# Performance work log

Hardware: AMD Instinct MI355X
Metric: run time of the kernel (lower is better)

## Reference

```python
import jax, jax.numpy as jnp
import numpy as np

B, C_IN, IMG = 16, 3, 224
P = 8                      # patch size (kernel == stride)
D = 256                    # d_model == embed_dim
NH = 8                     # num heads
HD = D // NH               # head dim = 32
G = IMG // P               # 28x28 patch grid
N = G * G                  # 784 patches
MRD = 31                   # max_relative_dist
T = 2 * MRD - 1            # 61
SCALE = HD ** -0.5


def setup_inputs() -> dict:
    key = jax.random.key(0)
    ks = jax.random.split(key, 11)
    std = 0.02
    yy, xx = jnp.meshgrid(jnp.arange(G), jnp.arange(G), indexing='ij')
    pos = jnp.stack([yy.ravel(), xx.ravel()], axis=-1).astype(jnp.int32)  # (N,2)
    return {
        'cur_frame': jax.random.normal(ks[0], (B, C_IN, IMG, IMG), jnp.float32),
        'prev_frame': jax.random.normal(ks[1], (B, C_IN, IMG, IMG), jnp.float32),
        'conv_w': jax.random.normal(ks[2], (D, C_IN, P, P), jnp.float32) * std,
        'conv_b': jnp.zeros((D,), jnp.float32),
        'q_w': jax.random.normal(ks[3], (D, D), jnp.float32) * std,
        'q_b': jnp.zeros((D,), jnp.float32),
        'kv_w': jax.random.normal(ks[4], (2 * D, D), jnp.float32) * std,
        'kv_b': jnp.zeros((2 * D,), jnp.float32),
        'proj_w': jax.random.normal(ks[5], (D, D), jnp.float32) * std,
        'proj_b': jnp.zeros((D,), jnp.float32),
        'bias_table': jax.random.normal(ks[6], (T * T, NH), jnp.float32) * std,
        'cur_pos': pos,
        'prev_pos': pos,
    }


def _patch_embed(x, w, b):
    # Conv2d with kernel==stride==P (non-overlapping patches)
    y = jax.lax.conv_general_dilated(
        x, w, window_strides=(P, P), padding='VALID',
        dimension_numbers=('NCHW', 'OIHW', 'NCHW'))
    y = y + b[None, :, None, None]
    Bb, Dd, h, wd = y.shape
    return y.reshape(Bb, Dd, h * wd).transpose(0, 2, 1)  # (B, N, D)


def reference(cur_frame, prev_frame, conv_w, conv_b, q_w, q_b, kv_w, kv_b,
              proj_w, proj_b, bias_table, cur_pos, prev_pos):
    cur = _patch_embed(cur_frame, conv_w, conv_b)    # (B, N, D)
    prev = _patch_embed(prev_frame, conv_w, conv_b)  # (B, N, D)

    q = (cur @ q_w.T + q_b).reshape(B, N, NH, HD).transpose(0, 2, 1, 3) * SCALE
    kv = prev @ kv_w.T + kv_b                        # (B, N, 2D)
    k = kv[..., :D].reshape(B, N, NH, HD).transpose(0, 2, 1, 3)
    v = kv[..., D:].reshape(B, N, NH, HD).transpose(0, 2, 1, 3)

    attn = jnp.einsum('bhqd,bhkd->bhqk', q, k)       # (B, NH, N, N)

    # relative position bias gather: idx = (dy+30)*61 + (dx+30)
    rel = cur_pos[:, None, :] - prev_pos[None, :, :]             # (N, N, 2)
    idx = (rel[..., 0] + (MRD - 1)) * T + (rel[..., 1] + (MRD - 1))
    bias = bias_table[idx].transpose(2, 0, 1)                    # (NH, N, N)

    attn = jax.nn.softmax(attn + bias[None], axis=-1)
    x = jnp.einsum('bhqk,bhkd->bqhd', attn, v).reshape(B, N, D)
    return x @ proj_w.T + proj_b
```

## Files before the change

### kernel.cpp

```cpp
#include <hip/hip_runtime.h>

#define B_ 16
#define NP 784
#define D_ 256
#define NH_ 8
#define HD_ 32
#define KEMB 192
#define SCALE_ 0.17677669529663687f
#define LOG2E_ 1.4426950408889634f

typedef __attribute__((ext_vector_type(4))) float f32x4;
typedef __attribute__((ext_vector_type(8))) short bf16x8;
typedef __attribute__((ext_vector_type(4))) short bf16x4;

__device__ __forceinline__ unsigned short f2bf(float f) {
    union { float f; unsigned int u; } v; v.f = f;
    unsigned int u = v.u;
    unsigned int r = (u + 0x7fffu + ((u >> 16) & 1u)) >> 16;
    return (unsigned short)r;
}

__device__ __forceinline__ unsigned int cvtpk(float a, float b) {
    unsigned int r;
    asm("v_cvt_pk_bf16_f32 %0, %1, %2" : "=v"(r) : "v"(a), "v"(b));
    return r;
}

__device__ __forceinline__ float fexp2(float x) {
#if __has_builtin(__builtin_amdgcn_exp2f)
    return __builtin_amdgcn_exp2f(x);
#else
    return exp2f(x);
#endif
}

__device__ __forceinline__ void gl_lds16(const unsigned short* g, unsigned short* l) {
    __builtin_amdgcn_global_load_lds(
        (const __attribute__((address_space(1))) unsigned int*)(const void*)g,
        (__attribute__((address_space(3))) unsigned int*)(void*)l, 16, 0, 0);
}

__global__ __launch_bounds__(256) void prep_k(
    const float* __restrict__ s0, const float* __restrict__ s1,
    const float* __restrict__ s2, const float* __restrict__ s3,
    unsigned short* __restrict__ d,
    const float* __restrict__ bt, float* __restrict__ bto)
{
    if (blockIdx.x < 304) {
        int i = (blockIdx.x * 256 + threadIdx.x) * 4;
        const float* s; int off;
        if (i < 49152)            { s = s0; off = i; }
        else if (i < 114688)      { s = s1; off = i - 49152; }
        else if (i < 245760)      { s = s2; off = i - 114688; }
        else if (i < 311296)      { s = s3; off = i - 245760; }
        else return;
        float4 v = *(const float4*)(s + off);
        unsigned short o0 = f2bf(v.x), o1 = f2bf(v.y), o2 = f2bf(v.z), o3 = f2bf(v.w);
        unsigned short* dst = d + i;
        dst[0] = o0; dst[1] = o1; dst[2] = o2; dst[3] = o3;
    } else {
        int i = (blockIdx.x - 304) * 256 + threadIdx.x;
        if (i < 29768) {
            int h = i / 3721, idx = i - h * 3721;
            bto[i] = bt[idx * NH_ + h] * LOG2E_;
        }
    }
}

__global__ __launch_bounds__(256) void gemm_conv(
    const float* __restrict__ cur, const float* __restrict__ prev,
    const unsigned short* __restrict__ W, const float* __restrict__ bias,
    unsigned short* __restrict__ outp)
{
    __shared__ __align__(16) unsigned short At[32 * 64];
    __shared__ __align__(16) unsigned short Bt[256 * 64];
    const int tid = threadIdx.x;
    const int lane = tid & 63, wid = tid >> 6;
    const int lo = lane & 15, hi = lane >> 4;
    const int m0 = blockIdx.x * 32;
    const int wvb = wid * 512;
    const float* asrc;
    unsigned short* adst;
    {
        int row = tid >> 3, seg = tid & 7;
        int m = m0 + row;
        int fb = m / NP, n = m - fb * NP;
        int py = n / 28, px = n - py * 28;
        const float* F = (fb >= 16 ? prev + (size_t)(fb - 16) * 150528 : cur + (size_t)fb * 150528);
        asrc = F + (py * 8 + seg) * 224 + px * 8;
        adst = At + row * 64 + ((seg ^ (row & 7)) * 8);
    }
    f32x4 acc[2][4] = {};
#pragma unroll
    for (int kt = 0; kt < 3; ++kt) {
        __syncthreads();
#pragma unroll
        for (int i = 0; i < 8; ++i) {
            int s = i * 256 + tid;
            int row = s >> 3, seg = (s & 7) ^ (row & 7);
            gl_lds16(W + (size_t)row * KEMB + kt * 64 + seg * 8, Bt + i * 2048 + wvb);
        }
        {
            const float* src = asrc + kt * 50176;
            float4 a0 = *(const float4*)(src);
            float4 a1 = *(const float4*)(src + 4);
            union { unsigned int u[4]; bf16x8 v; } ov;
            ov.u[0] = cvtpk(a0.x, a0.y); ov.u[1] = cvtpk(a0.z, a0.w);
            ov.u[2] = cvtpk(a1.x, a1.y); ov.u[3] = cvtpk(a1.z, a1.w);
            *(bf16x8*)(void*)(adst) = ov.v;
        }
        __syncthreads();
#pragma unroll
        for (int kk = 0; kk < 2; ++kk) {
            bf16x8 af[2], bfv[4];
#pragma unroll
            for (int f = 0; f < 2; ++f) {
                int rowa = f * 16 + lo;
                af[f] = *(const bf16x8*)(const void*)(At + rowa * 64 + (((kk * 4 + hi) ^ (rowa & 7)) * 8));
            }
#pragma unroll
            for (int f = 0; f < 4; ++f) {
                int rowb = wid * 64 + f * 16 + lo;
                bfv[f] = *(const bf16x8*)(const void*)(Bt + rowb * 64 + (((kk * 4 + hi) ^ (rowb & 7)) * 8));
            }
#pragma unroll
            for (int fr = 0; fr < 2; ++fr)
#pragma unroll
                for (int fc = 0; fc < 4; ++fc)
                    acc[fr][fc] = __builtin_amdgcn_mfma_f32_16x16x32_bf16(af[fr], bfv[fc], acc[fr][fc], 0, 0, 0);
        }
    }
#pragma unroll
    for (int fr = 0; fr < 2; ++fr)
#pragma unroll
        for (int fc = 0; fc < 4; ++fc)
#pragma unroll
            for (int r = 0; r < 4; ++r) {
                int m = m0 + fr * 16 + hi * 4 + r;
                int c = wid * 64 + fc * 16 + lo;
                outp[(size_t)m * D_ + c] = f2bf(acc[fr][fc][r] + bias[c]);
            }
}

__global__ __launch_bounds__(256) void gemm_qkv(
    const unsigned short* __restrict__ emb,
    const unsigned short* __restrict__ w_q, const float* __restrict__ q_b,
    const unsigned short* __restrict__ w_kv, const float* __restrict__ kv_b,
    unsigned short* __restrict__ q_h, unsigned short* __restrict__ k_h,
    unsigned short* __restrict__ v_t)
{
    __shared__ __align__(16) unsigned short At[128 * 64];
    __shared__ __align__(16) unsigned short Bt[128 * 64];
    const int tid = threadIdx.x;
    const int lo = tid & 15, hi = (tid >> 4) & 3, wid = tid >> 6;
    const int m0 = blockIdx.x * 128;
    const int y = blockIdx.y;
    const bool iskv = y >= 2;
    const unsigned short* Abase = iskv ? emb + (size_t)12544 * D_ : emb;
    const unsigned short* W = iskv ? w_kv : w_q;
    const float* bias = iskv ? kv_b : q_b;
    const int n0 = (iskv ? y - 2 : y) * 128;
    const int wr = wid >> 1, wc = wid & 1;
    const int wvb = wid * 512;
    f32x4 acc[4][4] = {};
#pragma unroll
    for (int kt = 0; kt < 4; ++kt) {
        const int k0 = kt * 64;
        __syncthreads();
#pragma unroll
        for (int i = 0; i < 4; ++i) {
            int s = i * 256 + tid;
            int row = s >> 3, seg = (s & 7) ^ (row & 7);
            gl_lds16(Abase + (size_t)(m0 + row) * D_ + k0 + seg * 8, At + i * 2048 + wvb);
            gl_lds16(W + (size_t)(n0 + row) * D_ + k0 + seg * 8, Bt + i * 2048 + wvb);
        }
        __syncthreads();
#pragma unroll
        for (int kk = 0; kk < 2; ++kk) {
            bf16x8 af[4], bfv[4];
#pragma unroll
            for (int f = 0; f < 4; ++f) {
                int rowa = wr * 64 + f * 16 + lo;
                af[f] = *(const bf16x8*)(const void*)(At + rowa * 64 + (((kk * 4 + hi) ^ (rowa & 7)) * 8));
                int rowb = wc * 64 + f * 16 + lo;
                bfv[f] = *(const bf16x8*)(const void*)(Bt + rowb * 64 + (((kk * 4 + hi) ^ (rowb & 7)) * 8));
            }
#pragma unroll
            for (int fr = 0; fr < 4; ++fr)
#pragma unroll
                for (int fc = 0; fc < 4; ++fc)
                    acc[fr][fc] = __builtin_amdgcn_mfma_f32_16x16x32_bf16(af[fr], bfv[fc], acc[fr][fc], 0, 0, 0);
        }
    }
#pragma unroll
    for (int fr = 0; fr < 4; ++fr)
#pragma unroll
        for (int fc = 0; fc < 4; ++fc)
#pragma unroll
            for (int r = 0; r < 4; ++r) {
                int m = m0 + wr * 64 + fr * 16 + hi * 4 + r;
                int c = n0 + wc * 64 + fc * 16 + lo;
                float val = acc[fr][fc][r] + bias[c];
                int b = m / NP, n = m - (m / NP) * NP;
                if (!iskv) {
                    int h = c >> 5, d = c & 31;
                    q_h[(((size_t)(b * NH_ + h)) * NP + n) * HD_ + d] = f2bf(val * (SCALE_ * LOG2E_));
                } else if (c < D_) {
                    int h = c >> 5, d = c & 31;
                    k_h[(((size_t)(b * NH_ + h)) * NP + n) * HD_ + d] = f2bf(val);
                } else {
                    int cc = c - D_; int h = cc >> 5, d = cc & 31;
                    v_t[(((size_t)(b * NH_ + h)) * HD_ + d) * NP + n] = f2bf(val);
                }
            }
}

__global__ __launch_bounds__(256) void gemm_px(
    const unsigned short* __restrict__ A, const unsigned short* __restrict__ W,
    const float* __restrict__ bias, float* __restrict__ outp)
{
    __shared__ __align__(16) unsigned short At[32 * 64];
    __shared__ __align__(16) unsigned short Bt[128 * 64];
    const int tid = threadIdx.x;
    const int lo = tid & 15, hi = (tid >> 4) & 3, wid = tid >> 6;
    const int m0 = blockIdx.x * 32, n0 = blockIdx.y * 128;
    const int wr = wid >> 1, wc = wid & 1;
    const int wvb = wid * 512;
    f32x4 acc[4] = {};
#pragma unroll
    for (int kt = 0; kt < 4; ++kt) {
        const int k0 = kt * 64;
        __syncthreads();
        {
            int row = tid >> 3, seg = (tid & 7) ^ ((tid >> 3) & 7);
            gl_lds16(A + (size_t)(m0 + row) * D_ + k0 + seg * 8, At + wvb);
        }
#pragma unroll
        for (int i = 0; i < 4; ++i) {
            int s = i * 256 + tid;
            int row = s >> 3, seg = (s & 7) ^ (row & 7);
            gl_lds16(W + (size_t)(n0 + row) * D_ + k0 + seg * 8, Bt + i * 2048 + wvb);
        }
        __syncthreads();
#pragma unroll
        for (int kk = 0; kk < 2; ++kk) {
            bf16x8 af, bfv[4];
            {
                int rowa = wr * 16 + lo;
                af = *(const bf16x8*)(const void*)(At + rowa * 64 + (((kk * 4 + hi) ^ (rowa & 7)) * 8));
            }
#pragma unroll
            for (int f = 0; f < 4; ++f) {
                int rowb = wc * 64 + f * 16 + lo;
                bfv[f] = *(const bf16x8*)(const void*)(Bt + rowb * 64 + (((kk * 4 + hi) ^ (rowb & 7)) * 8));
            }
#pragma unroll
            for (int fc = 0; fc < 4; ++fc)
                acc[fc] = __builtin_amdgcn_mfma_f32_16x16x32_bf16(af, bfv[fc], acc[fc], 0, 0, 0);
        }
    }
#pragma unroll
    for (int fc = 0; fc < 4; ++fc)
#pragma unroll
        for (int r = 0; r < 4; ++r) {
            int m = m0 + wr * 16 + hi * 4 + r;
            int c = n0 + wc * 64 + fc * 16 + lo;
            outp[(size_t)m * D_ + c] = acc[fc][r] + bias[c];
        }
}

__global__ __launch_bounds__(448) void attn_k(
    const unsigned short* __restrict__ qh, const unsigned short* __restrict__ kh,
    const unsigned short* __restrict__ vt, const float* __restrict__ bias_t,
    const int* __restrict__ cpos, const int* __restrict__ ppos,
    unsigned short* __restrict__ x)
{
    __shared__ __align__(16) unsigned short Vt[2][32 * 64];
    __shared__ __align__(16) float2 Bp[1890];
    __shared__ int ktab[196];
    const int tid = threadIdx.x;
    const int lane = tid & 63, wid = tid >> 6;
    const int lo = lane & 15, hi = lane >> 4;
    const int bid = blockIdx.x;
    const int h = bid & 7;
    const int t2 = bid >> 3;
    const int b = t2 / 7;
    const int qt = t2 - b * 7;
    const int bh = b * 8 + h;
    const int q0 = qt * 112 + wid * 16;
    const int blbase = (qt * 4 + 3) * 61;

    {
        const float* bsl = bias_t + h * 3721 + blbase;
        for (int i = tid; i < 1890; i += 448)
            Bp[i] = float2{ bsl[i], bsl[i + 1] };
        if (tid < 196) {
            int kc = tid * 4;
            ktab[tid] = ppos[2 * kc] * 61 + ppos[2 * kc + 1];
        }
    }

    bf16x8 qf;
    int qb;
    {
        int qr = q0 + lo;
        qf = *(const bf16x8*)(const void*)(qh + (((size_t)bh * NP) + qr) * HD_ + hi * 8);
        qb = cpos[qr * 2] * 61 + cpos[qr * 2 + 1] + 1860 - blbase;
    }

    const unsigned short* kbase = kh + (size_t)bh * NP * HD_;
    const unsigned short* vbase = vt + (size_t)bh * HD_ * NP;
    const int tv = tid - 192, sd = tv >> 3, ssg = tv & 7;
    bf16x8 vst = {};

    auto issue = [&](int kt) {
        if (tid >= 192)
            vst = *(const bf16x8*)(const void*)(vbase + sd * NP + kt * 64 + ssg * 8);
    };
    auto stage = [&](int buf) {
        if (tid >= 192) {
            int f = ssg >> 2;
            int j4 = ((ssg >> 1) & 1) * 4;
            int blkA = f * 4 + ((2 * ssg) & 3);
            int blkB = f * 4 + ((2 * ssg + 1) & 3);
            bf16x4 vlo = { vst[0], vst[1], vst[2], vst[3] };
            bf16x4 vhi = { vst[4], vst[5], vst[6], vst[7] };
            *(bf16x4*)(void*)(Vt[buf] + sd * 64 + ((blkA ^ (sd & 7)) * 8) + j4) = vlo;
            *(bf16x4*)(void*)(Vt[buf] + sd * 64 + ((blkB ^ (sd & 7)) * 8) + j4) = vhi;
        }
    };

    f32x4 o[2] = {};
    float lr = 0.f;

    issue(0);
    stage(0);
    for (int kt = 0; kt < 13; ++kt) {
        int cur = kt & 1;
        int k0 = kt * 64;
        if (kt < 12) issue(kt + 1);
        bf16x8 kf[4];
#pragma unroll
        for (int g = 0; g < 4; ++g)
            kf[g] = *(const bf16x8*)(const void*)(kbase + (size_t)(k0 + g * 16 + lo) * HD_ + hi * 8);
        __syncthreads();
        bool tail = (kt == 12);

        f32x4 bc[4];
#pragma unroll
        for (int g = 0; g < 4; ++g) {
            if (tail && g > 0) {
                bc[g] = f32x4{ -1e30f, -1e30f, -1e30f, -1e30f };
            } else {
                int kbg = ktab[kt * 16 + g * 4 + hi];
                int off = qb - kbg - 3;
                float2 pA = Bp[off];
                float2 pB = Bp[off + 2];
                bc[g][0] = pB.y; bc[g][1] = pB.x; bc[g][2] = pA.y; bc[g][3] = pA.x;
            }
        }
        f32x4 s[4];
#pragma unroll
        for (int g = 0; g < 4; ++g)
            s[g] = __builtin_amdgcn_mfma_f32_16x16x32_bf16(kf[g], qf, bc[g], 0, 0, 0);
        unsigned int c[4][2];
        float psum = 0.f;
#pragma unroll
        for (int g = 0; g < 4; ++g) {
            float p0 = fexp2(s[g][0]);
            float p1 = fexp2(s[g][1]);
            float p2 = fexp2(s[g][2]);
            float p3 = fexp2(s[g][3]);
            psum += (p0 + p1) + (p2 + p3);
            c[g][0] = cvtpk(p0, p1);
            c[g][1] = cvtpk(p2, p3);
        }
        lr += psum;
#pragma unroll
        for (int f = 0; f < 2; ++f) {
            union { unsigned int u[4]; bf16x8 v; } pu;
            pu.u[0] = c[2 * f][0]; pu.u[1] = c[2 * f][1];
            pu.u[2] = c[2 * f + 1][0]; pu.u[3] = c[2 * f + 1][1];
#pragma unroll
            for (int cc = 0; cc < 2; ++cc) {
                int d = cc * 16 + lo;
                bf16x8 vf = *(const bf16x8*)(const void*)(Vt[cur] + d * 64 + (((f * 4 + hi) ^ (d & 7)) * 8));
                o[cc] = __builtin_amdgcn_mfma_f32_16x16x32_bf16(pu.v, vf, o[cc], 0, 0, 0);
            }
        }
        if (kt < 12) stage(cur ^ 1);
    }
    lr += __shfl_xor(lr, 16);
    lr += __shfl_xor(lr, 32);
    float li = 1.0f / lr;
    float lro[4];
#pragma unroll
    for (int r = 0; r < 4; ++r)
        lro[r] = __shfl(li, (lane & 48) | (hi * 4 + r));
#pragma unroll
    for (int cc = 0; cc < 2; ++cc)
#pragma unroll
        for (int r = 0; r < 4; ++r) {
            int qr = q0 + hi * 4 + r;
            float val = o[cc][r] * lro[r];
            x[((size_t)b * NP + qr) * D_ + h * HD_ + cc * 16 + lo] = f2bf(val);
        }
}

extern "C" void kernel_launch(void* const* d_in, const int* in_sizes, int n_in,
                              void* d_out, int out_size, void* d_ws, size_t ws_size,
                              hipStream_t stream)
{
    const float* cur    = (const float*)d_in[0];
    const float* prev   = (const float*)d_in[1];
    const float* conv_w = (const float*)d_in[2];
    const float* conv_b = (const float*)d_in[3];
    const float* q_w    = (const float*)d_in[4];
    const float* q_b    = (const float*)d_in[5];
    const float* kv_w   = (const float*)d_in[6];
    const float* kv_b   = (const float*)d_in[7];
    const float* proj_w = (const float*)d_in[8];
    const float* proj_b = (const float*)d_in[9];
    const float* btab   = (const float*)d_in[10];
    const int* cpos     = (const int*)d_in[11];
    const int* ppos     = (const int*)d_in[12];

    char* ws = (char*)d_ws;
    unsigned short* w_conv = (unsigned short*)(ws + 0);
    unsigned short* w_q    = (unsigned short*)(ws + 98304);
    unsigned short* w_kv   = (unsigned short*)(ws + 229376);
    unsigned short* w_pr   = (unsigned short*)(ws + 491520);
    float* bias_t          = (float*)(ws + 622592);
    unsigned short* emb    = (unsigned short*)(ws + 10256384);
    unsigned short* q_h    = (unsigned short*)(ws + 23101440);
    unsigned short* k_h    = (unsigned short*)(ws + 29523968);
    unsigned short* v_t    = (unsigned short*)(ws + 35946496);
    unsigned short* xb     = (unsigned short*)(ws + 42369024);

    prep_k<<<421, 256, 0, stream>>>(conv_w, q_w, kv_w, proj_w, w_conv, btab, bias_t);
    gemm_conv<<<784, 256, 0, stream>>>(cur, prev, w_conv, conv_b, emb);
    gemm_qkv<<<dim3(98, 6), 256, 0, stream>>>(emb, w_q, q_b, w_kv, kv_b, q_h, k_h, v_t);
    attn_k<<<896, 448, 0, stream>>>(q_h, k_h, v_t, bias_t, cpos, ppos, xb);
    gemm_px<<<dim3(392, 2), 256, 0, stream>>>(xb, w_pr, proj_b, (float*)d_out);

    (void)in_sizes; (void)n_in; (void)out_size; (void)ws_size;
}
```

Before: 78.87 us.

## Fuse patch-embed conv GEMM with Q/KV projection via LDS-resident embedding tile

Merges the conv patch-embedding GEMM and the Q/KV projection GEMM into one kernel. Each 32-row block keeps its bf16 embedding tile in shared memory and immediately multiplies it by the Q or KV weights, which are read directly from global memory. This removes the emb round-trip through HBM and one kernel launch. In exchange, the 32-row tiles reuse weights less, weight fragments are loaded uncached from global memory inside the MFMA loop, and prev-frame blocks do twice the work of cur-frame blocks, creating load imbalance.

```diff
diff --git a/kernel.cpp b/kernel.cpp
--- a/kernel.cpp
+++ b/kernel.cpp
@@ -67,10 +67,13 @@
     }
 }
 
-__global__ __launch_bounds__(256) void gemm_conv(
+__global__ __launch_bounds__(256) void conv_qkv(
     const float* __restrict__ cur, const float* __restrict__ prev,
-    const unsigned short* __restrict__ W, const float* __restrict__ bias,
-    unsigned short* __restrict__ outp)
+    const unsigned short* __restrict__ W, const float* __restrict__ cbias,
+    const unsigned short* __restrict__ w_q, const float* __restrict__ q_b,
+    const unsigned short* __restrict__ w_kv, const float* __restrict__ kv_b,
+    unsigned short* __restrict__ q_h, unsigned short* __restrict__ k_h,
+    unsigned short* __restrict__ v_t)
 {
     __shared__ __align__(16) unsigned short At[32 * 64];
     __shared__ __align__(16) unsigned short Bt[256 * 64];
@@ -130,89 +133,79 @@
                     acc[fr][fc] = __builtin_amdgcn_mfma_f32_16x16x32_bf16(af[fr], bfv[fc], acc[fr][fc], 0, 0, 0);
         }
     }
+    __syncthreads();
+    unsigned short* Et = Bt;
 #pragma unroll
     for (int fr = 0; fr < 2; ++fr)
 #pragma unroll
         for (int fc = 0; fc < 4; ++fc)
 #pragma unroll
             for (int r = 0; r < 4; ++r) {
-                int m = m0 + fr * 16 + hi * 4 + r;
-                int c = wid * 64 + fc * 16 + lo;
-                outp[(size_t)m * D_ + c] = f2bf(acc[fr][fc][r] + bias[c]);
-            }
-}
-
-__global__ __launch_bounds__(256) void gemm_qkv(
-    const unsigned short* __restrict__ emb,
-    const unsigned short* __restrict__ w_q, const float* __restrict__ q_b,
-    const unsigned short* __restrict__ w_kv, const float* __restrict__ kv_b,
-    unsigned short* __restrict__ q_h, unsigned short* __restrict__ k_h,
-    unsigned short* __restrict__ v_t)
-{
-    __shared__ __align__(16) unsigned short At[128 * 64];
-    __shared__ __align__(16) unsigned short Bt[128 * 64];
-    const int tid = threadIdx.x;
-    const int lo = tid & 15, hi = (tid >> 4) & 3, wid = tid >> 6;
-    const int m0 = blockIdx.x * 128;
-    const int y = blockIdx.y;
-    const bool iskv = y >= 2;
-    const unsigned short* Abase = iskv ? emb + (size_t)12544 * D_ : emb;
-    const unsigned short* W = iskv ? w_kv : w_q;
-    const float* bias = iskv ? kv_b : q_b;
-    const int n0 = (iskv ? y - 2 : y) * 128;
-    const int wr = wid >> 1, wc = wid & 1;
-    const int wvb = wid * 512;
-    f32x4 acc[4][4] = {};
-#pragma unroll
-    for (int kt = 0; kt < 4; ++kt) {
-        const int k0 = kt * 64;
-        __syncthreads();
-#pragma unroll
-        for (int i = 0; i < 4; ++i) {
-            int s = i * 256 + tid;
-            int row = s >> 3, seg = (s & 7) ^ (row & 7);
-            gl_lds16(Abase + (size_t)(m0 + row) * D_ + k0 + seg * 8, At + i * 2048 + wvb);
-            gl_lds16(W + (size_t)(n0 + row) * D_ + k0 + seg * 8, Bt + i * 2048 + wvb);
-        }
-        __syncthreads();
-#pragma unroll
-        for (int kk = 0; kk < 2; ++kk) {
-            bf16x8 af[4], bfv[4];
-#pragma unroll
-            for (int f = 0; f < 4; ++f) {
-                int rowa = wr * 64 + f * 16 + lo;
-                af[f] = *(const bf16x8*)(const void*)(At + rowa * 64 + (((kk * 4 + hi) ^ (rowa & 7)) * 8));
-                int rowb = wc * 64 + f * 16 + lo;
-                bfv[f] = *(const bf16x8*)(const void*)(Bt + rowb * 64 + (((kk * 4 + hi) ^ (rowb & 7)) * 8));
-            }
-#pragma unroll
-            for (int fr = 0; fr < 4; ++fr)
-#pragma unroll
-                for (int fc = 0; fc < 4; ++fc)
-                    acc[fr][fc] = __builtin_amdgcn_mfma_f32_16x16x32_bf16(af[fr], bfv[fc], acc[fr][fc], 0, 0, 0);
-        }
-    }
-#pragma unroll
-    for (int fr = 0; fr < 4; ++fr)
-#pragma unroll
-        for (int fc = 0; fc < 4; ++fc)
-#pragma unroll
-            for (int r = 0; r < 4; ++r) {
-                int m = m0 + wr * 64 + fr * 16 + hi * 4 + r;
-                int c = n0 + wc * 64 + fc * 16 + lo;
-                float val = acc[fr][fc][r] + bias[c];
-                int b = m / NP, n = m - (m / NP) * NP;
-                if (!iskv) {
-                    int h = c >> 5, d = c & 31;
-                    q_h[(((size_t)(b * NH_ + h)) * NP + n) * HD_ + d] = f2bf(val * (SCALE_ * LOG2E_));
-                } else if (c < D_) {
-                    int h = c >> 5, d = c & 31;
-                    k_h[(((size_t)(b * NH_ + h)) * NP + n) * HD_ + d] = f2bf(val);
-                } else {
-                    int cc = c - D_; int h = cc >> 5, d = cc & 31;
-                    v_t[(((size_t)(b * NH_ + h)) * HD_ + d) * NP + n] = f2bf(val);
+                int row = fr * 16 + hi * 4 + r;
+                int w = fc * 16 + lo;
+                int seg = w >> 3, el = w & 7;
+                Et[row * 256 + wid * 64 + ((seg ^ (row & 7)) << 3) + el] =
+                    f2bf(acc[fr][fc][r] + cbias[wid * 64 + w]);
+            }
+    __syncthreads();
+
+    const bool isprev = (blockIdx.x >= 392);
+    const unsigned short* Wb = isprev ? w_kv : w_q;
+    const float* bb = isprev ? kv_b : q_b;
+    const int NWF = isprev ? 8 : 4;
+    const int nbase = wid * (NWF * 16);
+    f32x4 a2[2][8];
+#pragma unroll
+    for (int i = 0; i < 2; ++i)
+#pragma unroll
+        for (int j = 0; j < 8; ++j)
+            a2[i][j] = f32x4{0.f, 0.f, 0.f, 0.f};
+#pragma unroll
+    for (int kk = 0; kk < 8; ++kk) {
+        bf16x8 af2[2];
+#pragma unroll
+        for (int mf = 0; mf < 2; ++mf) {
+            int m = mf * 16 + lo;
+            af2[mf] = *(const bf16x8*)(const void*)(
+                Et + m * 256 + (kk >> 1) * 64 + (((((kk & 1) << 2) + hi) ^ (m & 7)) << 3));
+        }
+#pragma unroll
+        for (int nf = 0; nf < 8; ++nf) {
+            if (nf < NWF) {
+                bf16x8 bv = *(const bf16x8*)(const void*)(
+                    Wb + (size_t)(nbase + nf * 16 + lo) * D_ + kk * 32 + hi * 8);
+                a2[0][nf] = __builtin_amdgcn_mfma_f32_16x16x32_bf16(af2[0], bv, a2[0][nf], 0, 0, 0);
+                a2[1][nf] = __builtin_amdgcn_mfma_f32_16x16x32_bf16(af2[1], bv, a2[1][nf], 0, 0, 0);
+            }
+        }
+    }
+#pragma unroll
+    for (int mf = 0; mf < 2; ++mf)
+#pragma unroll
+        for (int nf = 0; nf < 8; ++nf) {
+            if (nf < NWF) {
+#pragma unroll
+                for (int r = 0; r < 4; ++r) {
+                    int mg = m0 + mf * 16 + hi * 4 + r;
+                    int c = nbase + nf * 16 + lo;
+                    float val = a2[mf][nf][r] + bb[c];
+                    int bq = mg / NP, n = mg - bq * NP;
+                    if (!isprev) {
+                        int hh = c >> 5, dd = c & 31;
+                        q_h[(((size_t)(bq * NH_ + hh)) * NP + n) * HD_ + dd] = f2bf(val * (SCALE_ * LOG2E_));
+                    } else {
+                        int bp = bq - 16;
+                        if (c < D_) {
+                            int hh = c >> 5, dd = c & 31;
+                            k_h[(((size_t)(bp * NH_ + hh)) * NP + n) * HD_ + dd] = f2bf(val);
+                        } else {
+                            int cc = c - D_; int hh = cc >> 5, dd = cc & 31;
+                            v_t[(((size_t)(bp * NH_ + hh)) * HD_ + dd) * NP + n] = f2bf(val);
+                        }
+                    }
                 }
             }
+        }
 }
 
 __global__ __launch_bounds__(256) void gemm_px(
@@ -431,15 +424,14 @@
     unsigned short* w_kv   = (unsigned short*)(ws + 229376);
     unsigned short* w_pr   = (unsigned short*)(ws + 491520);
     float* bias_t          = (float*)(ws + 622592);
-    unsigned short* emb    = (unsigned short*)(ws + 10256384);
     unsigned short* q_h    = (unsigned short*)(ws + 23101440);
     unsigned short* k_h    = (unsigned short*)(ws + 29523968);
     unsigned short* v_t    = (unsigned short*)(ws + 35946496);
     unsigned short* xb     = (unsigned short*)(ws + 42369024);
 
     prep_k<<<421, 256, 0, stream>>>(conv_w, q_w, kv_w, proj_w, w_conv, btab, bias_t);
-    gemm_conv<<<784, 256, 0, stream>>>(cur, prev, w_conv, conv_b, emb);
-    gemm_qkv<<<dim3(98, 6), 256, 0, stream>>>(emb, w_q, q_b, w_kv, kv_b, q_h, k_h, v_t);
+    conv_qkv<<<784, 256, 0, stream>>>(cur, prev, w_conv, conv_b,
+                                      w_q, q_b, w_kv, kv_b, q_h, k_h, v_t);
     attn_k<<<896, 448, 0, stream>>>(q_h, k_h, v_t, bias_t, cpos, ppos, xb);
     gemm_px<<<dim3(392, 2), 256, 0, stream>>>(xb, w_pr, proj_b, (float*)d_out);
 
```

New measurement: 94.61 us. +20.0%, slower.

## Fuse weight prep into conv kernel and convert conv weights on the fly

Applied to the files above, without the earlier changes.

Merges the separate weight/bias-table prep kernel into the patch-embedding conv kernel. Extra blocks handle the q/kv/proj bf16 conversion and the bias-table transpose, which removes one launch and the dependency between them. The conv blocks now read fp32 conv weights and convert them to bf16 in registers before writing to LDS, replacing the async global-to-LDS copy of pre-converted weights. The cost is more global traffic and conversion work per conv block, since every block re-converts the same 192x256 weights.

```diff
diff --git a/kernel.cpp b/kernel.cpp
--- a/kernel.cpp
+++ b/kernel.cpp
@@ -40,45 +40,42 @@
         (__attribute__((address_space(3))) unsigned int*)(void*)l, 16, 0, 0);
 }
 
-__global__ __launch_bounds__(256) void prep_k(
-    const float* __restrict__ s0, const float* __restrict__ s1,
-    const float* __restrict__ s2, const float* __restrict__ s3,
-    unsigned short* __restrict__ d,
-    const float* __restrict__ bt, float* __restrict__ bto)
-{
-    if (blockIdx.x < 304) {
-        int i = (blockIdx.x * 256 + threadIdx.x) * 4;
-        const float* s; int off;
-        if (i < 49152)            { s = s0; off = i; }
-        else if (i < 114688)      { s = s1; off = i - 49152; }
-        else if (i < 245760)      { s = s2; off = i - 114688; }
-        else if (i < 311296)      { s = s3; off = i - 245760; }
-        else return;
-        float4 v = *(const float4*)(s + off);
-        unsigned short o0 = f2bf(v.x), o1 = f2bf(v.y), o2 = f2bf(v.z), o3 = f2bf(v.w);
-        unsigned short* dst = d + i;
-        dst[0] = o0; dst[1] = o1; dst[2] = o2; dst[3] = o3;
-    } else {
-        int i = (blockIdx.x - 304) * 256 + threadIdx.x;
-        if (i < 29768) {
-            int h = i / 3721, idx = i - h * 3721;
-            bto[i] = bt[idx * NH_ + h] * LOG2E_;
-        }
-    }
-}
-
-__global__ __launch_bounds__(256) void gemm_conv(
+__global__ __launch_bounds__(256) void conv_prep(
     const float* __restrict__ cur, const float* __restrict__ prev,
-    const unsigned short* __restrict__ W, const float* __restrict__ bias,
+    const float* __restrict__ conv_w32, const float* __restrict__ bias,
+    const float* __restrict__ q_w32, const float* __restrict__ kv_w32,
+    const float* __restrict__ pr_w32,
+    unsigned short* __restrict__ w_q, unsigned short* __restrict__ w_kv,
+    unsigned short* __restrict__ w_pr,
+    const float* __restrict__ bt, float* __restrict__ bto,
     unsigned short* __restrict__ outp)
 {
+    const int tid = threadIdx.x;
+    if (blockIdx.x >= 784) {
+        int bi = blockIdx.x - 784;
+        if (bi < 256) {
+            int i = (bi * 256 + tid) * 4;
+            const float* s; unsigned short* dp; int off;
+            if (i < 65536)       { s = q_w32;  dp = w_q;  off = i; }
+            else if (i < 196608) { s = kv_w32; dp = w_kv; off = i - 65536; }
+            else                 { s = pr_w32; dp = w_pr; off = i - 196608; }
+            float4 v = *(const float4*)(s + off);
+            dp[off + 0] = f2bf(v.x); dp[off + 1] = f2bf(v.y);
+            dp[off + 2] = f2bf(v.z); dp[off + 3] = f2bf(v.w);
+        } else {
+            int i = (bi - 256) * 256 + tid;
+            if (i < 29768) {
+                int h = i / 3721, idx = i - h * 3721;
+                bto[i] = bt[idx * NH_ + h] * LOG2E_;
+            }
+        }
+        return;
+    }
     __shared__ __align__(16) unsigned short At[32 * 64];
     __shared__ __align__(16) unsigned short Bt[256 * 64];
-    const int tid = threadIdx.x;
     const int lane = tid & 63, wid = tid >> 6;
     const int lo = lane & 15, hi = lane >> 4;
     const int m0 = blockIdx.x * 32;
-    const int wvb = wid * 512;
     const float* asrc;
     unsigned short* adst;
     {
@@ -97,8 +94,14 @@
 #pragma unroll
         for (int i = 0; i < 8; ++i) {
             int s = i * 256 + tid;
-            int row = s >> 3, seg = (s & 7) ^ (row & 7);
-            gl_lds16(W + (size_t)row * KEMB + kt * 64 + seg * 8, Bt + i * 2048 + wvb);
+            int row = s >> 3, j = s & 7, seg = j ^ (row & 7);
+            const float* wsrc = conv_w32 + row * KEMB + kt * 64 + seg * 8;
+            float4 b0 = *(const float4*)(wsrc);
+            float4 b1 = *(const float4*)(wsrc + 4);
+            union { unsigned int u[4]; bf16x8 v; } bv;
+            bv.u[0] = cvtpk(b0.x, b0.y); bv.u[1] = cvtpk(b0.z, b0.w);
+            bv.u[2] = cvtpk(b1.x, b1.y); bv.u[3] = cvtpk(b1.z, b1.w);
+            *(bf16x8*)(void*)(Bt + row * 64 + j * 8) = bv.v;
         }
         {
             const float* src = asrc + kt * 50176;
@@ -426,7 +429,6 @@
     const int* ppos     = (const int*)d_in[12];
 
     char* ws = (char*)d_ws;
-    unsigned short* w_conv = (unsigned short*)(ws + 0);
     unsigned short* w_q    = (unsigned short*)(ws + 98304);
     unsigned short* w_kv   = (unsigned short*)(ws + 229376);
     unsigned short* w_pr   = (unsigned short*)(ws + 491520);
@@ -437,8 +439,9 @@
     unsigned short* v_t    = (unsigned short*)(ws + 35946496);
     unsigned short* xb     = (unsigned short*)(ws + 42369024);
 
-    prep_k<<<421, 256, 0, stream>>>(conv_w, q_w, kv_w, proj_w, w_conv, btab, bias_t);
-    gemm_conv<<<784, 256, 0, stream>>>(cur, prev, w_conv, conv_b, emb);
+    conv_prep<<<1157, 256, 0, stream>>>(cur, prev, conv_w, conv_b,
+                                        q_w, kv_w, proj_w, w_q, w_kv, w_pr,
+                                        btab, bias_t, emb);
     gemm_qkv<<<dim3(98, 6), 256, 0, stream>>>(emb, w_q, q_b, w_kv, kv_b, q_h, k_h, v_t);
     attn_k<<<896, 448, 0, stream>>>(q_h, k_h, v_t, bias_t, cpos, ppos, xb);
     gemm_px<<<dim3(392, 2), 256, 0, stream>>>(xb, w_pr, proj_b, (float*)d_out);
```

Result: no change. 77.46 us (-1.8%).
